# Kernel tuning notes

Measured on AMD Instinct MI355X. Metric: run time of the kernel, lower is better.

Reference implementation:

```python
import jax, jax.numpy as jnp
import numpy as np

N = 100000   # nodes
E = 1000000  # edges
F_IN = 64    # num_node_features
H = 64       # hidden_channels
G = 64       # graphs in batch
OUT = 1


def setup_inputs() -> dict:
    key = jax.random.key(0)
    ks = jax.random.split(key, 16)
    inp = {}
    inp['x'] = jax.random.normal(ks[0], (N, F_IN), dtype=jnp.float32)
    inp['edge_index'] = jax.random.randint(ks[1], (2, E), 0, N, dtype=jnp.int64)
    inp['batch'] = jnp.sort(jax.random.randint(ks[2], (N,), 0, G, dtype=jnp.int64))
    s_in = 1.0 / np.sqrt(F_IN)
    s_h = 1.0 / np.sqrt(H)
    # GraphConv 1: in=F_IN -> H  (lin_rel has bias, lin_root has no bias)
    inp['W1r'] = jax.random.uniform(ks[3], (F_IN, H), jnp.float32, -s_in, s_in)
    inp['b1'] = jax.random.uniform(ks[4], (H,), jnp.float32, -s_in, s_in)
    inp['W1o'] = jax.random.uniform(ks[5], (F_IN, H), jnp.float32, -s_in, s_in)
    # GraphConv 2, 3: H -> H
    inp['W2r'] = jax.random.uniform(ks[6], (H, H), jnp.float32, -s_h, s_h)
    inp['b2'] = jax.random.uniform(ks[7], (H,), jnp.float32, -s_h, s_h)
    inp['W2o'] = jax.random.uniform(ks[8], (H, H), jnp.float32, -s_h, s_h)
    inp['W3r'] = jax.random.uniform(ks[9], (H, H), jnp.float32, -s_h, s_h)
    inp['b3'] = jax.random.uniform(ks[10], (H,), jnp.float32, -s_h, s_h)
    inp['W3o'] = jax.random.uniform(ks[11], (H, H), jnp.float32, -s_h, s_h)
    # PReLU slopes (num_parameters=1, init=0.25)
    inp['a1'] = jnp.array(0.25, dtype=jnp.float32)
    inp['a2'] = jnp.array(0.25, dtype=jnp.float32)
    # head
    inp['W_lin0'] = jax.random.uniform(ks[12], (H, H), jnp.float32, -s_h, s_h)
    inp['b_lin0'] = jax.random.uniform(ks[13], (H,), jnp.float32, -s_h, s_h)
    inp['W_lin1'] = jax.random.uniform(ks[14], (H, OUT), jnp.float32, -s_h, s_h)
    inp['b_lin1'] = jax.random.uniform(ks[15], (OUT,), jnp.float32, -s_h, s_h)
    return inp


def _graph_conv(x, src, dst, Wr, b, Wo):
    # PyG GraphConv, aggr='add': out_i = Wr @ (sum_{j->i} x_j) + Wo @ x_i + b.
    # Aggregate raw features first (linear commutes with sum) -> one small GEMM.
    agg = jax.ops.segment_sum(x[src], dst, num_segments=N)  # [N, d_in]
    return agg @ Wr + x @ Wo + b


def _prelu(x, a):
    return jnp.where(x >= 0, x, a * x)


def reference(x, edge_index, batch, W1r, b1, W1o, W2r, b2, W2o, W3r, b3, W3o,
              a1, a2, W_lin0, b_lin0, W_lin1, b_lin1):
    src, dst = edge_index[0], edge_index[1]
    h = _graph_conv(x, src, dst, W1r, b1, W1o)
    h = _prelu(h, a1)  # dropout is identity in eval mode
    h = _graph_conv(h, src, dst, W2r, b2, W2o)
    h = _prelu(h, a2)
    h = _graph_conv(h, src, dst, W3r, b3, W3o)
    # global_mean_pool over graph ids
    sums = jax.ops.segment_sum(h, batch, num_segments=G)            # [G, H]
    cnts = jax.ops.segment_sum(jnp.ones((N,), h.dtype), batch, num_segments=G)
    pooled = sums / jnp.maximum(cnts, 1.0)[:, None]
    out = pooled @ W_lin0 + b_lin0
    out = out @ W_lin1 + b_lin1
    return out  # [G, OUT]
```

## Files before the change

### kernel.cpp

```cpp
#include <hip/hip_runtime.h>

#define FDIM 64
#define ECAP 512
#define NBK_SHIFT 8
#define BCAP 4096
#define CHUNK 4096

typedef unsigned int uint32;
typedef unsigned short ushort16;
typedef __attribute__((ext_vector_type(8))) short bf8v;
typedef __attribute__((ext_vector_type(4))) float f4v;

static inline size_t align_up(size_t v) { return (v + 255) & ~(size_t)255; }

__device__ __forceinline__ float bcastf(float v, int l) {
    return __int_as_float(__builtin_amdgcn_readlane(__float_as_int(v), l));
}
__device__ __forceinline__ float bf_lo(uint32 u) { return __uint_as_float(u << 16); }
__device__ __forceinline__ float bf_hi(uint32 u) { return __uint_as_float(u & 0xFFFF0000u); }
__device__ __forceinline__ unsigned short f2bf(float f) {
    uint32 u = __float_as_uint(f);
    return (unsigned short)((u + 0x7FFFu + ((u >> 16) & 1u)) >> 16);
}
__device__ __forceinline__ float bf2f(unsigned short s) {
    return __uint_as_float(((uint32)s) << 16);
}


__global__ __launch_bounds__(256) void k_bhist(const int* __restrict__ dst,
                                               int* __restrict__ bcount, int E, int nb,
                                               const float* __restrict__ xin,
                                               ushort16* __restrict__ xbf, long n4) {
    __shared__ int h[512];
    for (int i = threadIdx.x; i < nb; i += 256) h[i] = 0;
    __syncthreads();
    long stride = (long)gridDim.x * blockDim.x;
    long tid = (long)blockIdx.x * blockDim.x + threadIdx.x;
    for (long i = tid; i < n4; i += stride) {
        float4 v = ((const float4*)xin)[i];
        uint2 o;
        o.x = (uint32)f2bf(v.x) | ((uint32)f2bf(v.y) << 16);
        o.y = (uint32)f2bf(v.z) | ((uint32)f2bf(v.w) << 16);
        ((uint2*)xbf)[i] = o;
    }
    for (long e = tid; e < E; e += stride)
        atomicAdd(&h[dst[e] >> NBK_SHIFT], 1);
    __syncthreads();
    for (int i = threadIdx.x; i < nb; i += 256)
        if (h[i]) atomicAdd(&bcount[i], h[i]);
}

__global__ __launch_bounds__(512) void k_bscan(const int* __restrict__ bcount,
                                               int* __restrict__ bbase,
                                               int* __restrict__ bcursor, int nb,
                                               int* __restrict__ rowstart, int n, int E) {
    __shared__ int sh[512];
    int t = threadIdx.x;
    int v = (t < nb) ? bcount[t] : 0;
    sh[t] = v;
    __syncthreads();
    for (int off = 1; off < 512; off <<= 1) {
        int a = (t >= off) ? sh[t - off] : 0;
        __syncthreads();
        sh[t] += a;
        __syncthreads();
    }
    if (t < nb) { int ex = sh[t] - v; bbase[t] = ex; bcursor[t] = ex; }
    if (t == 0) { bbase[nb] = E; rowstart[n] = E; }
}

__global__ __launch_bounds__(1024) void k_bgroup(const int* __restrict__ src,
                                                 const int* __restrict__ dst,
                                                 int* __restrict__ bcursor,
                                                 uint32* __restrict__ ebuf, int E, int nb) {
    __shared__ uint32 sorted[CHUNK];
    __shared__ unsigned short bop[CHUNK];
    __shared__ int hist[512];
    __shared__ int gbase[512];
    __shared__ int cur[512];
    __shared__ int sh[512];
    int c0 = blockIdx.x * CHUNK;
    int cend = c0 + CHUNK; if (cend > E) cend = E;
    int cnt = cend - c0;
    int t = threadIdx.x;
    for (int i = t; i < nb; i += 1024) hist[i] = 0;
    __syncthreads();
    for (int i = t; i < cnt; i += 1024)
        atomicAdd(&hist[dst[c0 + i] >> NBK_SHIFT], 1);
    __syncthreads();
    int v = 0;
    if (t < 512) { v = (t < nb) ? hist[t] : 0; sh[t] = v; }
    __syncthreads();
    for (int off = 1; off < 512; off <<= 1) {
        int a = (t >= off && t < 512) ? sh[t - off] : 0;
        __syncthreads();
        if (t < 512) sh[t] += a;
        __syncthreads();
    }
    if (t < nb) {
        int lofs = sh[t] - v;
        cur[t] = lofs;
        hist[t] = lofs;
        gbase[t] = v ? atomicAdd(&bcursor[t], v) : 0;
    }
    __syncthreads();
    for (int i = t; i < cnt; i += 1024) {
        int d = dst[c0 + i], s = src[c0 + i];
        int b = d >> NBK_SHIFT;
        int p = atomicAdd(&cur[b], 1);
        sorted[p] = ((uint32)(d & ((1 << NBK_SHIFT) - 1)) << 24) | (uint32)s;
        bop[p] = (unsigned short)b;
    }
    __syncthreads();
    for (int i = t; i < cnt; i += 1024) {
        int b = bop[i];
        ebuf[gbase[b] + (i - hist[b])] = sorted[i];
    }
}

__global__ __launch_bounds__(512) void k_blocal(const uint32* __restrict__ ebuf,
                                                const int* __restrict__ bbase,
                                                int* __restrict__ rowstart,
                                                int* __restrict__ adj, int n) {
    __shared__ uint32 raw[BCAP];
    __shared__ int srt[BCAP];
    __shared__ int hist[257];
    __shared__ int cur[256];
    int b = blockIdx.x;
    int t = threadIdx.x;
    int lo = bbase[b], hi = bbase[b + 1];
    int cnt = hi - lo;
    for (int i = t; i < 257; i += 512) hist[i] = 0;
    __syncthreads();
    if (cnt <= BCAP) {
        for (int i = t; i < cnt; i += 512) {
            uint32 v = ebuf[lo + i];
            raw[i] = v;
            atomicAdd(&hist[(v >> 24) + 1], 1);
        }
        __syncthreads();
        for (int off = 1; off < 256; off <<= 1) {
            int a = (t >= off && t < 256) ? hist[t + 1 - off] : 0;
            __syncthreads();
            if (t < 256) hist[t + 1] += a;
            __syncthreads();
        }
        if (t < 256) cur[t] = hist[t];
        __syncthreads();
        for (int i = t; i < cnt; i += 512) {
            uint32 v = raw[i];
            int p = atomicAdd(&cur[v >> 24], 1);
            srt[p] = (int)(v & 0xFFFFFF);
        }
        __syncthreads();
        for (int i = t; i < cnt; i += 512) adj[lo + i] = srt[i];
    } else {
        for (int i = t; i < cnt; i += 512) {
            uint32 v = ebuf[lo + i];
            atomicAdd(&hist[(v >> 24) + 1], 1);
        }
        __syncthreads();
        for (int off = 1; off < 256; off <<= 1) {
            int a = (t >= off && t < 256) ? hist[t + 1 - off] : 0;
            __syncthreads();
            if (t < 256) hist[t + 1] += a;
            __syncthreads();
        }
        if (t < 256) cur[t] = hist[t];
        __syncthreads();
        for (int i = t; i < cnt; i += 512) {
            uint32 v = ebuf[lo + i];
            int p = atomicAdd(&cur[v >> 24], 1);
            adj[lo + p] = (int)(v & 0xFFFFFF);
        }
    }
    if (t < 256) {
        int node = (b << NBK_SHIFT) + t;
        if (node < n) rowstart[node] = lo + hist[t];
    }
}


template<int DO_POOL>
__global__ __launch_bounds__(1024) void k_layer(
    const ushort16* __restrict__ Hbf, const int* __restrict__ rowstart,
    const int* __restrict__ adj, const float* __restrict__ Wr,
    const float* __restrict__ Wo, const float* __restrict__ bias,
    const float* __restrict__ slope_p, ushort16* __restrict__ HbfOut,
    int n, int do_prelu, const int* __restrict__ batch, float* __restrict__ sums)
{
    __shared__ unsigned short wh[64 * 128];
    __shared__ unsigned short wl[64 * 128];
    __shared__ int eidx[16][ECAP];

    for (int e = threadIdx.x; e < 64 * 128; e += 1024) {
        int nn = e >> 7;
        int k  = e & 127;
        float v = (k < 64) ? Wr[k * 64 + nn] : Wo[(k - 64) * 64 + nn];
        unsigned short hi = f2bf(v);
        unsigned short lo = f2bf(v - bf2f(hi));
        int boff = nn * 256 + ((k * 2) ^ ((nn & 7) << 4));
        wh[boff >> 1] = hi;
        wl[boff >> 1] = lo;
    }
    __syncthreads();

    int lane  = threadIdx.x & 63;
    int l15   = lane & 15;
    int kg    = lane >> 4;
    int koff  = kg * 8;
    int wslot = threadIdx.x >> 6;
    int wid  = (blockIdx.x * blockDim.x + threadIdx.x) >> 6;
    int nw   = (gridDim.x * blockDim.x) >> 6;
    int ntiles = (n + 15) >> 4;
    float slope = do_prelu ? slope_p[0] : 1.0f;
    float bv0 = bias[l15], bv1 = bias[16 + l15], bv2 = bias[32 + l15], bv3 = bias[48 + l15];

    for (int t = wid; t < ntiles; t += nw) {
        int base16 = t * 16;
        int node = base16 + l15;
        bool valid = node < n;
        int s0 = valid ? rowstart[node] : 0;
        int s1 = valid ? rowstart[node + 1] : 0;
        int ebase = __builtin_amdgcn_readlane(s0, 0);
        int eend  = __builtin_amdgcn_readlane(s1, 15);
        if (!valid) { s0 = 0; s1 = 0; }
        if (base16 + 16 > n) eend = rowstart[n];
        int ecount = eend - ebase;

        int cap = ecount < ECAP ? ecount : ECAP;
        for (int i = lane; i < cap; i += 64) eidx[wslot][i] = adj[ebase + i];
        asm volatile("s_waitcnt lgkmcnt(0)" ::: "memory");

        int4 su = {0, 0, 0, 0}, sv = {0, 0, 0, 0};
        if (valid) {
            const ushort16* sp = Hbf + ((long)node << 6);
            su = *(const int4*)(sp + koff);
            sv = *(const int4*)(sp + koff + 32);
        }

        float acc[16];
#pragma unroll
        for (int i = 0; i < 16; i++) acc[i] = 0.f;

#define ACC8(UU, BASE) \
        acc[BASE+0] += bf_lo(UU.x); acc[BASE+1] += bf_hi(UU.x); \
        acc[BASE+2] += bf_lo(UU.y); acc[BASE+3] += bf_hi(UU.y); \
        acc[BASE+4] += bf_lo(UU.z); acc[BASE+5] += bf_hi(UU.z); \
        acc[BASE+6] += bf_lo(UU.w); acc[BASE+7] += bf_hi(UU.w);

        if (ecount <= ECAP) {
            int ls0 = s0 - ebase, ls1 = s1 - ebase;
            const int* ix = eidx[wslot];
            int j = ls0;
            for (; j + 4 <= ls1; j += 4) {
                long r0 = ix[j], r1 = ix[j + 1], r2 = ix[j + 2], r3 = ix[j + 3];
                const ushort16* p0 = Hbf + (r0 << 6);
                const ushort16* p1 = Hbf + (r1 << 6);
                const ushort16* p2 = Hbf + (r2 << 6);
                const ushort16* p3 = Hbf + (r3 << 6);
                int4 u0 = *(const int4*)(p0 + koff), v0 = *(const int4*)(p0 + koff + 32);
                int4 u1 = *(const int4*)(p1 + koff), v1 = *(const int4*)(p1 + koff + 32);
                int4 u2 = *(const int4*)(p2 + koff), v2 = *(const int4*)(p2 + koff + 32);
                int4 u3 = *(const int4*)(p3 + koff), v3 = *(const int4*)(p3 + koff + 32);
                ACC8(u0, 0)  ACC8(u1, 0)  ACC8(u2, 0)  ACC8(u3, 0)
                ACC8(v0, 8)  ACC8(v1, 8)  ACC8(v2, 8)  ACC8(v3, 8)
            }
            for (; j < ls1; j++) {
                long r0 = ix[j];
                const ushort16* p0 = Hbf + (r0 << 6);
                int4 u0 = *(const int4*)(p0 + koff), v0 = *(const int4*)(p0 + koff + 32);
                ACC8(u0, 0)  ACC8(v0, 8)
            }
        } else {
            for (int e = s0; e < s1; e++) {
                long r0 = adj[e];
                const ushort16* p0 = Hbf + (r0 << 6);
                int4 u0 = *(const int4*)(p0 + koff), v0 = *(const int4*)(p0 + koff + 32);
                ACC8(u0, 0)  ACC8(v0, 8)
            }
        }
#undef ACC8

        bf8v ah[4], al[2];
#pragma unroll
        for (int kb = 0; kb < 2; kb++) {
#pragma unroll
            for (int j = 0; j < 8; j++) {
                float v = acc[kb * 8 + j];
                unsigned short h = f2bf(v);
                ah[kb][j] = (short)h;
                al[kb][j] = (short)f2bf(v - bf2f(h));
            }
        }
        ah[2] = __builtin_bit_cast(bf8v, su);
        ah[3] = __builtin_bit_cast(bf8v, sv);

        f4v C[4];
        C[0] = (f4v){bv0, bv0, bv0, bv0};
        C[1] = (f4v){bv1, bv1, bv1, bv1};
        C[2] = (f4v){bv2, bv2, bv2, bv2};
        C[3] = (f4v){bv3, bv3, bv3, bv3};

#pragma unroll
        for (int kb = 0; kb < 4; kb++) {
#pragma unroll
            for (int nt = 0; nt < 4; nt++) {
                int row = nt * 16 + l15;
                int boff = row * 256 + (((kb * 32 + kg * 8) * 2) ^ ((l15 & 7) << 4));
                bf8v bh = *(const bf8v*)((const char*)wh + boff);
                bf8v bl = *(const bf8v*)((const char*)wl + boff);
                C[nt] = __builtin_amdgcn_mfma_f32_16x16x32_bf16(ah[kb], bh, C[nt], 0, 0, 0);
                if (kb < 2)
                    C[nt] = __builtin_amdgcn_mfma_f32_16x16x32_bf16(al[kb], bh, C[nt], 0, 0, 0);
                C[nt] = __builtin_amdgcn_mfma_f32_16x16x32_bf16(ah[kb], bl, C[nt], 0, 0, 0);
            }
        }

        if (!DO_POOL) {
#pragma unroll
            for (int r = 0; r < 4; r++) {
                int onode = base16 + kg * 4 + r;
                if (onode < n) {
#pragma unroll
                    for (int nt = 0; nt < 4; nt++) {
                        float v = C[nt][r];
                        v = v >= 0.f ? v : slope * v;
                        HbfOut[((long)onode << 6) + nt * 16 + l15] = f2bf(v);
                    }
                }
            }
        } else {
            int curg = -1;
            float a0 = 0.f, a1 = 0.f, a2 = 0.f, a3 = 0.f;
#pragma unroll
            for (int r = 0; r < 4; r++) {
                int onode = base16 + kg * 4 + r;
                if (onode < n) {
                    int g = batch[onode];
                    if (g != curg) {
                        if (curg >= 0) {
                            atomicAdd(&sums[curg * FDIM +  0 + l15], a0);
                            atomicAdd(&sums[curg * FDIM + 16 + l15], a1);
                            atomicAdd(&sums[curg * FDIM + 32 + l15], a2);
                            atomicAdd(&sums[curg * FDIM + 48 + l15], a3);
                        }
                        curg = g; a0 = a1 = a2 = a3 = 0.f;
                    }
                    a0 += C[0][r]; a1 += C[1][r]; a2 += C[2][r]; a3 += C[3][r];
                }
            }
            if (curg >= 0) {
                atomicAdd(&sums[curg * FDIM +  0 + l15], a0);
                atomicAdd(&sums[curg * FDIM + 16 + l15], a1);
                atomicAdd(&sums[curg * FDIM + 32 + l15], a2);
                atomicAdd(&sums[curg * FDIM + 48 + l15], a3);
            }
        }
    }
}


__global__ __launch_bounds__(64) void k_head(const float* __restrict__ sums,
                                             const int* __restrict__ batch, int n,
                                             const float* __restrict__ W0,
                                             const float* __restrict__ b0,
                                             const float* __restrict__ W1,
                                             const float* __restrict__ b1,
                                             float* __restrict__ out, int OUT) {
    int g = blockIdx.x;
    int lane = threadIdx.x;
    int lo = 0, hi = n;
    while (lo < hi) { int m = (lo + hi) >> 1; if (batch[m] < g) lo = m + 1; else hi = m; }
    int lo2 = lo, hi2 = n;
    while (lo2 < hi2) { int m = (lo2 + hi2) >> 1; if (batch[m] <= g) lo2 = m + 1; else hi2 = m; }
    float c = (float)(lo2 - lo);
    if (c < 1.f) c = 1.f;
    float p = sums[g * FDIM + lane] / c;

    float h0 = 0.f, h1 = 0.f, h2 = 0.f, h3 = 0.f;
#pragma unroll
    for (int k = 0; k < FDIM; k += 4) {
        h0 += bcastf(p, k + 0) * W0[(k + 0) * FDIM + lane];
        h1 += bcastf(p, k + 1) * W0[(k + 1) * FDIM + lane];
        h2 += bcastf(p, k + 2) * W0[(k + 2) * FDIM + lane];
        h3 += bcastf(p, k + 3) * W0[(k + 3) * FDIM + lane];
    }
    float hid = b0[lane] + ((h0 + h1) + (h2 + h3));
    for (int o = 0; o < OUT; o++) {
        float part = hid * W1[lane * OUT + o];
#pragma unroll
        for (int m = 32; m >= 1; m >>= 1) part += __shfl_xor(part, m, 64);
        if (lane == 0) out[g * OUT + o] = part + b1[o];
    }
}

extern "C" void kernel_launch(void* const* d_in, const int* in_sizes, int n_in,
                              void* d_out, int out_size, void* d_ws, size_t ws_size,
                              hipStream_t stream) {
    const float* x     = (const float*)d_in[0];
    const int*   ei    = (const int*)d_in[1];
    const int*   batch = (const int*)d_in[2];
    const float* W1r = (const float*)d_in[3];
    const float* b1  = (const float*)d_in[4];
    const float* W1o = (const float*)d_in[5];
    const float* W2r = (const float*)d_in[6];
    const float* b2  = (const float*)d_in[7];
    const float* W2o = (const float*)d_in[8];
    const float* W3r = (const float*)d_in[9];
    const float* b3  = (const float*)d_in[10];
    const float* W3o = (const float*)d_in[11];
    const float* a1  = (const float*)d_in[12];
    const float* a2  = (const float*)d_in[13];
    const float* Wl0 = (const float*)d_in[14];
    const float* bl0 = (const float*)d_in[15];
    const float* Wl1 = (const float*)d_in[16];
    const float* bl1 = (const float*)d_in[17];

    int N = in_sizes[0] / FDIM;
    int E = in_sizes[1] / 2;
    int OUT = in_sizes[17];
    int G = out_size / OUT;
    int nb = (N + 255) >> NBK_SHIFT;

    const int* src = ei;
    const int* dst = ei + E;

    char* w = (char*)d_ws;
    int* rowstart = (int*)w;              w += align_up((size_t)(N + 1) * 4);
    int* adj      = (int*)w;              w += align_up((size_t)E * 4 + 256);
    uint32* ebuf  = (uint32*)w;           w += align_up((size_t)E * 4);
    int* bbase    = (int*)w;              w += align_up((size_t)(nb + 1) * 4);
    int* bcursor  = (int*)w;              w += align_up((size_t)nb * 4);
    ushort16* xbf = (ushort16*)w;         w += align_up((size_t)N * FDIM * 2);
    ushort16* hb1 = (ushort16*)w;         w += align_up((size_t)N * FDIM * 2);
    ushort16* hb2 = (ushort16*)w;         w += align_up((size_t)N * FDIM * 2);
    char* zbase   = w;
    int* bcount   = (int*)w;              w += align_up(512 * 4);
    float* sums   = (float*)w;            w += align_up((size_t)G * FDIM * 4);

    hipMemsetAsync(zbase, 0, (size_t)(w - zbase), stream);

    k_bhist<<<512, 256, 0, stream>>>(dst, bcount, E, nb, x, xbf, (long)N * FDIM / 4);
    k_bscan<<<1, 512, 0, stream>>>(bcount, bbase, bcursor, nb, rowstart, N, E);
    int nchunks = (E + CHUNK - 1) / CHUNK;
    k_bgroup<<<nchunks, 1024, 0, stream>>>(src, dst, bcursor, ebuf, E, nb);
    k_blocal<<<nb, 512, 0, stream>>>(ebuf, bbase, rowstart, adj, N);

    int ntiles = (N + 15) / 16;
    int layerGrid = (ntiles + 15) / 16;
    k_layer<0><<<layerGrid, 1024, 0, stream>>>(xbf, rowstart, adj, W1r, W1o, b1, a1, hb1, N, 1, nullptr, nullptr);
    k_layer<0><<<layerGrid, 1024, 0, stream>>>(hb1, rowstart, adj, W2r, W2o, b2, a2, hb2, N, 1, nullptr, nullptr);
    k_layer<1><<<layerGrid, 1024, 0, stream>>>(hb2, rowstart, adj, W3r, W3o, b3, nullptr, hb1, N, 0, batch, sums);

    k_head<<<G, 64, 0, stream>>>(sums, batch, N, Wl0, bl0, Wl1, bl1, (float*)d_out, OUT);
}
```

Measured before the change: 235.8 us.

## Split mean-pool out of last GraphConv layer into a dedicated chunked pooling kernel

Removes the fused pooling path from the third layer kernel. That layer now writes its bf16 output like the other layers, and a new k_pool kernel sums rows over 32-node chunks per wave before doing atomics into the per-graph sums. The aim is far fewer global float atomics on the small G×64 sums array, whose contention is high in the fused epilogue. In exchange it adds a full bf16 write and re-read of the layer-3 activations, an extra launch, and bf16 rounding of the values before pooling.

```diff
diff --git a/kernel.cpp b/kernel.cpp
--- a/kernel.cpp
+++ b/kernel.cpp
@@ -1,6 +1,7 @@
 #include <hip/hip_runtime.h>
 
 #define FDIM 64
+#define POOL_CHUNK 32
 #define ECAP 512
 #define NBK_SHIFT 8
 #define BCAP 4096
@@ -181,13 +182,12 @@
 }
 
 
-template<int DO_POOL>
 __global__ __launch_bounds__(1024) void k_layer(
     const ushort16* __restrict__ Hbf, const int* __restrict__ rowstart,
     const int* __restrict__ adj, const float* __restrict__ Wr,
     const float* __restrict__ Wo, const float* __restrict__ bias,
     const float* __restrict__ slope_p, ushort16* __restrict__ HbfOut,
-    int n, int do_prelu, const int* __restrict__ batch, float* __restrict__ sums)
+    int n, int do_prelu)
 {
     __shared__ unsigned short wh[64 * 128];
     __shared__ unsigned short wl[64 * 128];
@@ -317,47 +317,44 @@
             }
         }
 
-        if (!DO_POOL) {
-#pragma unroll
-            for (int r = 0; r < 4; r++) {
-                int onode = base16 + kg * 4 + r;
-                if (onode < n) {
-#pragma unroll
-                    for (int nt = 0; nt < 4; nt++) {
-                        float v = C[nt][r];
-                        v = v >= 0.f ? v : slope * v;
-                        HbfOut[((long)onode << 6) + nt * 16 + l15] = f2bf(v);
-                    }
+#pragma unroll
+        for (int r = 0; r < 4; r++) {
+            int onode = base16 + kg * 4 + r;
+            if (onode < n) {
+#pragma unroll
+                for (int nt = 0; nt < 4; nt++) {
+                    float v = C[nt][r];
+                    v = v >= 0.f ? v : slope * v;
+                    HbfOut[((long)onode << 6) + nt * 16 + l15] = f2bf(v);
                 }
             }
-        } else {
-            int curg = -1;
-            float a0 = 0.f, a1 = 0.f, a2 = 0.f, a3 = 0.f;
-#pragma unroll
-            for (int r = 0; r < 4; r++) {
-                int onode = base16 + kg * 4 + r;
-                if (onode < n) {
-                    int g = batch[onode];
-                    if (g != curg) {
-                        if (curg >= 0) {
-                            atomicAdd(&sums[curg * FDIM +  0 + l15], a0);
-                            atomicAdd(&sums[curg * FDIM + 16 + l15], a1);
-                            atomicAdd(&sums[curg * FDIM + 32 + l15], a2);
-                            atomicAdd(&sums[curg * FDIM + 48 + l15], a3);
-                        }
-                        curg = g; a0 = a1 = a2 = a3 = 0.f;
-                    }
-                    a0 += C[0][r]; a1 += C[1][r]; a2 += C[2][r]; a3 += C[3][r];
-                }
-            }
-            if (curg >= 0) {
-                atomicAdd(&sums[curg * FDIM +  0 + l15], a0);
-                atomicAdd(&sums[curg * FDIM + 16 + l15], a1);
-                atomicAdd(&sums[curg * FDIM + 32 + l15], a2);
-                atomicAdd(&sums[curg * FDIM + 48 + l15], a3);
-            }
-        }
-    }
+        }
+    }
+}
+
+
+__global__ __launch_bounds__(256) void k_pool(const ushort16* __restrict__ h,
+                                              const int* __restrict__ batch,
+                                              float* __restrict__ sums, int n) {
+    int wave = (blockIdx.x * 256 + threadIdx.x) >> 6;
+    int lane = threadIdx.x & 63;
+    int start = wave * POOL_CHUNK;
+    if (start >= n) return;
+    int end = start + POOL_CHUNK;
+    if (end > n) end = n;
+    int cur = batch[start];
+    float acc = 0.f;
+#pragma unroll 4
+    for (int i = start; i < end; i++) {
+        int g = batch[i];
+        if (g != cur) {
+            atomicAdd(&sums[cur * FDIM + lane], acc);
+            acc = 0.f;
+            cur = g;
+        }
+        acc += bf2f(h[(long)i * FDIM + lane]);
+    }
+    atomicAdd(&sums[cur * FDIM + lane], acc);
 }
 
 
@@ -449,9 +446,12 @@
 
     int ntiles = (N + 15) / 16;
     int layerGrid = (ntiles + 15) / 16;
-    k_layer<0><<<layerGrid, 1024, 0, stream>>>(xbf, rowstart, adj, W1r, W1o, b1, a1, hb1, N, 1, nullptr, nullptr);
-    k_layer<0><<<layerGrid, 1024, 0, stream>>>(hb1, rowstart, adj, W2r, W2o, b2, a2, hb2, N, 1, nullptr, nullptr);
-    k_layer<1><<<layerGrid, 1024, 0, stream>>>(hb2, rowstart, adj, W3r, W3o, b3, nullptr, hb1, N, 0, batch, sums);
-
+    k_layer<<<layerGrid, 1024, 0, stream>>>(xbf, rowstart, adj, W1r, W1o, b1, a1, hb1, N, 1);
+    k_layer<<<layerGrid, 1024, 0, stream>>>(hb1, rowstart, adj, W2r, W2o, b2, a2, hb2, N, 1);
+    k_layer<<<layerGrid, 1024, 0, stream>>>(hb2, rowstart, adj, W3r, W3o, b3, nullptr, hb1, N, 0);
+
+    int poolWaves = (N + POOL_CHUNK - 1) / POOL_CHUNK;
+    int poolGrid = (poolWaves + 3) / 4;
+    k_pool<<<poolGrid, 256, 0, stream>>>(hb1, batch, sums, N);
     k_head<<<G, 64, 0, stream>>>(sums, batch, N, Wl0, bl0, Wl1, bl1, (float*)d_out, OUT);
 }
```

After: 192.3 us, median of 2. 18.4% less time.
